# Kernel tuning notes

Measured on AMD Instinct MI355X. Metric: run time of the kernel, lower is better.

The kernel has to match this reference:

```python
import jax, jax.numpy as jnp
import numpy as np

B, T, C, N = 4, 12, 64, 10000
H = 64            # d_inner (GRU hidden)
L = 2             # num_layers
NE = 2000         # number of static hyperedges
NNZ = 80000       # incidence list length
TOPK = 10         # HGCNADP_topk
DE = 16           # HGCNADP_embed_dims
RATE = 0.5        # hyperedge_rate (blend static vs adaptive)


def setup_inputs() -> dict:
    key = jax.random.key(0)
    ks = jax.random.split(key, 10)
    scale = 0.05
    x = jax.random.normal(ks[0], (B, T, C, N), jnp.float32)
    node_idx = jax.random.randint(ks[1], (NNZ,), 0, N, jnp.int32)
    edge_idx = jax.random.randint(ks[2], (NNZ,), 0, NE, jnp.int32)
    hyperedge_index = jnp.stack([node_idx, edge_idx])  # (2, NNZ)
    node_embs = jax.random.normal(ks[3], (L, N, DE), jnp.float32) * 0.1
    W_zr = jax.random.normal(ks[4], (L, C + H, 2 * H), jnp.float32) * scale
    b_zr = jnp.zeros((L, 2 * H), jnp.float32)
    W_c = jax.random.normal(ks[5], (L, C + H, H), jnp.float32) * scale
    b_c = jnp.zeros((L, H), jnp.float32)
    W_out = jax.random.normal(ks[6], (L, H, C), jnp.float32) * scale
    b_out = jnp.zeros((L, C), jnp.float32)
    return {"x": x, "hyperedge_index": hyperedge_index, "node_embs": node_embs,
            "W_zr": W_zr, "b_zr": b_zr, "W_c": W_c, "b_c": b_c,
            "W_out": W_out, "b_out": b_out}


def reference(x, hyperedge_index, node_embs, W_zr, b_zr, W_c, b_c, W_out, b_out):
    # x: (B, T, C, N). Dropout is identity (eval mode).
    node_idx = hyperedge_index[0]
    edge_idx = hyperedge_index[1]
    edge_deg = jnp.zeros((NE,), x.dtype).at[edge_idx].add(1.0)
    inv_e = 1.0 / jnp.maximum(edge_deg, 1.0)
    node_deg = jnp.zeros((N,), x.dtype).at[node_idx].add(1.0)
    inv_n = 1.0 / jnp.maximum(node_deg, 1.0)

    def conv(f, topk_idx, topk_w):
        # f: (B, N, D). Static hypergraph pass: node -> hyperedge -> node.
        msg = jnp.take(f, node_idx, axis=1)                       # (B, NNZ, D)
        eagg = jnp.zeros((f.shape[0], NE, f.shape[2]), f.dtype).at[:, edge_idx].add(msg)
        eagg = eagg * inv_e[None, :, None]                        # (B, NE, D)
        stat = jnp.zeros_like(f).at[:, node_idx].add(jnp.take(eagg, edge_idx, axis=1))
        stat = stat * inv_n[None, :, None]                        # (B, N, D)
        # Adaptive top-k hyperedge aggregation (softmax-weighted neighbor sum).
        adp = jnp.einsum('bnkd,nk->bnd', jnp.take(f, topk_idx, axis=1), topk_w)
        return RATE * stat + (1.0 - RATE) * adp

    out = x
    for l in range(L):
        xl = out.transpose(0, 1, 3, 2)                            # (B, T, N, C)
        E = node_embs[l]
        scores = jax.nn.relu(E @ E.T)                             # (N, N)
        vals, idx = jax.lax.top_k(scores, TOPK)                   # (N, K)
        w = jax.nn.softmax(vals, axis=-1)
        Wz, bz = W_zr[l], b_zr[l]
        Wc_, bc_ = W_c[l], b_c[l]
        Wo, bo = W_out[l], b_out[l]

        def step(h, x_t):
            zr = jax.nn.sigmoid(conv(jnp.concatenate([x_t, h], -1), idx, w) @ Wz + bz)
            z, r = jnp.split(zr, 2, axis=-1)
            c = jnp.tanh(conv(jnp.concatenate([x_t, r * h], -1), idx, w) @ Wc_ + bc_)
            h_new = z * h + (1.0 - z) * c
            return h_new, h_new @ Wo + bo

        h0 = jnp.zeros((out.shape[0], N, H), x.dtype)
        _, ys = jax.lax.scan(step, h0, xl.transpose(1, 0, 2, 3))  # ys: (T, B, N, C)
        out = out + ys.transpose(1, 0, 3, 2)                      # residual, back to (B,T,C,N)
    return out
```

## Files before the change

kernel.cpp:

```cpp
#include <hip/hip_runtime.h>
#include <hip/hip_fp16.h>
#include <cstdio>

#define BB 4
#define TT 12
#define CC 64
#define NN 10000
#define HH 64
#define LL 2
#define NEDGE 2000
#define NNZT 80000
#define KTOP 10
#define DEMB 16
#define BT (BB*TT)

typedef long long ll;
typedef unsigned long long u64;
typedef unsigned int u32;
typedef unsigned short ushort;

typedef short bf16x8 __attribute__((ext_vector_type(8)));
typedef float f32x4 __attribute__((ext_vector_type(4)));

__device__ __forceinline__ void up8(const uint4 v, float* f) {
  const __half2* p = reinterpret_cast<const __half2*>(&v);
  float2 t0 = __half22float2(p[0]);
  float2 t1 = __half22float2(p[1]);
  float2 t2 = __half22float2(p[2]);
  float2 t3 = __half22float2(p[3]);
  f[0]=t0.x; f[1]=t0.y; f[2]=t1.x; f[3]=t1.y;
  f[4]=t2.x; f[5]=t2.y; f[6]=t3.x; f[7]=t3.y;
}
__device__ __forceinline__ uint4 pk8(const float* f) {
  __half2 h0 = __floats2half2_rn(f[0], f[1]);
  __half2 h1 = __floats2half2_rn(f[2], f[3]);
  __half2 h2 = __floats2half2_rn(f[4], f[5]);
  __half2 h3 = __floats2half2_rn(f[6], f[7]);
  uint4 r;
  r.x = *reinterpret_cast<unsigned*>(&h0);
  r.y = *reinterpret_cast<unsigned*>(&h1);
  r.z = *reinterpret_cast<unsigned*>(&h2);
  r.w = *reinterpret_cast<unsigned*>(&h3);
  return r;
}
__device__ __forceinline__ ushort f2bf(float x) {
  u32 u = __float_as_uint(x);
  u32 r = u + 0x7FFFu + ((u >> 16) & 1u);
  return (ushort)(r >> 16);
}
__device__ __forceinline__ uint4 pk8bf(const float* f) {
  uint4 r;
  r.x = (u32)f2bf(f[0]) | ((u32)f2bf(f[1])<<16);
  r.y = (u32)f2bf(f[2]) | ((u32)f2bf(f[3])<<16);
  r.z = (u32)f2bf(f[4]) | ((u32)f2bf(f[5])<<16);
  r.w = (u32)f2bf(f[6]) | ((u32)f2bf(f[7])<<16);
  return r;
}

__global__ void deg_kernel(const int* __restrict__ nidx, const int* __restrict__ eidx,
                           int* __restrict__ ndeg, int* __restrict__ edeg) {
  int i = blockIdx.x*256 + threadIdx.x;
  if (i < NNZT) { atomicAdd(&ndeg[nidx[i]],1); atomicAdd(&edeg[eidx[i]],1); }
}

__global__ void exscan_kernel(const int* __restrict__ cnt, int* __restrict__ off, int n) {
  __shared__ int part[256];
  int tid = threadIdx.x;
  int chunk = (n + 255)/256;
  int lo = tid*chunk, hi = min(lo+chunk, n);
  int s = 0;
  for (int i=lo; i<hi; ++i) s += cnt[i];
  part[tid]=s; __syncthreads();
  if (tid==0){ int acc=0; for(int i=0;i<256;++i){int v=part[i];part[i]=acc;acc+=v;} off[n]=acc; }
  __syncthreads();
  int acc = part[tid];
  for (int i=lo; i<hi; ++i){ off[i]=acc; acc+=cnt[i]; }
}

__global__ void fill_csr_kernel(const int* __restrict__ nidx, const int* __restrict__ eidx,
                                const int* __restrict__ noff, const int* __restrict__ eoff,
                                int* __restrict__ ncur, int* __restrict__ ecur,
                                int* __restrict__ node_edges, int* __restrict__ edge_nodes) {
  int i = blockIdx.x*256 + threadIdx.x;
  if (i >= NNZT) return;
  int n = nidx[i], e = eidx[i];
  int pn = atomicAdd(&ncur[n],1);
  node_edges[noff[n]+pn] = e;
  int pe = atomicAdd(&ecur[e],1);
  edge_nodes[eoff[e]+pe] = n;
}

__global__ void invdeg_kernel(const int* __restrict__ ndeg, const int* __restrict__ edeg,
                              float* __restrict__ inv_n, float* __restrict__ inv_e) {
  int i = blockIdx.x*256+threadIdx.x;
  if (i < NN) inv_n[i] = 1.0f/fmaxf((float)ndeg[i],1.0f);
  if (i < NEDGE) inv_e[i] = 1.0f/fmaxf((float)edeg[i],1.0f);
}

__global__ void prep_w_kernel(const float* __restrict__ W_zr, const float* __restrict__ W_c,
                              const float* __restrict__ W_o,
                              short* __restrict__ Wz_swb, short* __restrict__ Wc_swb,
                              short* __restrict__ Wo_swb) {
  int l = blockIdx.y;
  const float* Wz = W_zr + (size_t)l*128*128;
  const float* Wc = W_c  + (size_t)l*128*64;
  const float* Wo = W_o  + (size_t)l*64*64;
  short* Wz_sw = Wz_swb + (size_t)l*16384;
  short* Wc_sw = Wc_swb + (size_t)l*8192;
  short* Wo_sw = Wo_swb + (size_t)l*4096;
  int idx = blockIdx.x*256 + threadIdx.x;
  if (idx < 16384) {
    int i = idx&7, lane = (idx>>3)&63, kk = (idx>>9)&3, tc = idx>>11;
    int k = kk*32 + (lane>>4)*8 + i, col = tc*16 + (lane&15);
    Wz_sw[idx] = (short)f2bf(Wz[k*128+col]);
  }
  if (idx < 8192) {
    int i = idx&7, lane = (idx>>3)&63, kk = (idx>>9)&3, tc = idx>>11;
    int k = kk*32 + (lane>>4)*8 + i, col = tc*16 + (lane&15);
    Wc_sw[idx] = (short)f2bf(Wc[k*64+col]);
  }
  if (idx < 4096) {
    int i = idx&7, lane = (idx>>3)&63, kk = (idx>>9)&1, tc = idx>>10;
    int k = kk*32 + (lane>>4)*8 + i, col = tc*16 + (lane&15);
    Wo_sw[idx] = (short)f2bf(Wo[k*64+col]);
  }
}

__device__ __forceinline__ u64 sortstep(u64 X, int j, bool dir, int lane) {
  u64 p = __shfl_xor(X, j);
  bool lower = ((lane & j) == 0);
  bool keep_min = (dir == lower);
  bool xlt = (X < p);
  u64 mn = xlt ? X : p;
  u64 mx = xlt ? p : X;
  return keep_min ? mn : mx;
}

__device__ __forceinline__ void reselect(u64* bq, u64& thr, int& cnt, int lane) {
  int tot = 10 + cnt;
  u64 A = (lane < tot)      ? bq[lane]      : 0ull;
  u64 B = (lane + 64 < tot) ? bq[lane + 64] : 0ull;
  for (int k = 2; k <= 32; k <<= 1) {
    for (int j = k >> 1; j >= 1; j >>= 1) {
      bool dir = ((lane & k) == 0);
      A = sortstep(A, j, dir, lane);
      B = sortstep(B, j, dir, lane);
    }
  }
  for (int j = 32; j >= 1; j >>= 1) {
    A = sortstep(A, j, true,  lane);
    B = sortstep(B, j, false, lane);
  }
  {
    bool lt = (A < B);
    u64 mn = lt ? A : B, mx = lt ? B : A;
    A = mn; B = mx;
  }
  for (int j = 32; j >= 1; j >>= 1) {
    A = sortstep(A, j, true, lane);
    B = sortstep(B, j, true, lane);
  }
  if (lane >= 54) bq[63 - lane] = B;
  thr = __shfl(B, 54);
  cnt = 0;
}

__global__ void __launch_bounds__(256) topk_kernel(const float* __restrict__ embs,
                                                   int* __restrict__ tk_idx_b,
                                                   float* __restrict__ tk_w_b) {
  __shared__ u64 buf[16][128];
  const float* E = embs + (ll)blockIdx.y*NN*DEMB;
  int* tk_idx = tk_idx_b + (ll)blockIdx.y*NN*KTOP;
  float* tk_w = tk_w_b + (ll)blockIdx.y*NN*KTOP;
  int tid = threadIdx.x;
  int wv = tid >> 6, lane = tid & 63;
  int qbase = blockIdx.x*16 + wv*4;
  const float4* E4 = (const float4*)E;
  float4 q[4][4];
  #pragma unroll
  for (int u=0;u<4;++u) {
    int n = qbase + u;
    #pragma unroll
    for (int j=0;j<4;++j) q[u][j] = E4[(ll)n*4 + j];
  }
  u64 thr[4] = {0,0,0,0};
  int cnt[4] = {0,0,0,0};
  buf[tid>>4][tid&15] = 0ull;
  for (int cb=0; cb<NN; cb+=64) {
    int cand = cb + lane;
    bool valid = (cand < NN);
    int ca = valid ? cand : 0;
    float4 a0 = E4[(ll)ca*4], a1 = E4[(ll)ca*4+1], a2 = E4[(ll)ca*4+2], a3 = E4[(ll)ca*4+3];
    u64 low = (u64)(0x00FFFFFFu - (unsigned)cand);
    u64 key[4];
    #pragma unroll
    for (int u=0;u<4;++u) {
      float dot = q[u][0].x*a0.x + q[u][0].y*a0.y + q[u][0].z*a0.z + q[u][0].w*a0.w
                + q[u][1].x*a1.x + q[u][1].y*a1.y + q[u][1].z*a1.z + q[u][1].w*a1.w
                + q[u][2].x*a2.x + q[u][2].y*a2.y + q[u][2].z*a2.z + q[u][2].w*a2.w
                + q[u][3].x*a3.x + q[u][3].y*a3.y + q[u][3].z*a3.z + q[u][3].w*a3.w;
      float s = fmaxf(dot, 0.f);
      u64 kk = ((u64)__float_as_uint(s) << 32) | low;
      key[u] = valid ? kk : 0ull;
    }
    #pragma unroll
    for (int u=0;u<4;++u) {
      u64 mask = __ballot(key[u] > thr[u]);
      if (mask) {
        if (key[u] > thr[u]) {
          int myofs = (int)__popcll(mask & ((1ull<<lane)-1ull));
          buf[wv*4+u][10 + cnt[u] + myofs] = key[u];
        }
        cnt[u] += (int)__popcll(mask);
        if (cnt[u] >= 40) reselect(&buf[wv*4+u][0], thr[u], cnt[u], lane);
      }
    }
  }
  #pragma unroll
  for (int u=0;u<4;++u) {
    u64* bq = &buf[wv*4+u][0];
    if (cnt[u] > 0) reselect(bq, thr[u], cnt[u], lane);
    u64 k10 = (lane < 10) ? bq[lane] : 0ull;
    float v = __uint_as_float((unsigned)(k10 >> 32));
    int idx = 0x00FFFFFF - (int)(k10 & 0xFFFFFFFFull);
    float v0 = __shfl(v, 0);
    float e = (lane < 10) ? expf(v - v0) : 0.f;
    float s = e;
    for (int o=1;o<16;o<<=1) s += __shfl_xor(s, o);
    if (lane < 10) {
      int n = qbase + u;
      tk_w[n*KTOP + lane] = e / s;
      tk_idx[n*KTOP + lane] = idx;
    }
  }
}

__global__ void transpose_kernel(const float* __restrict__ src, __half* __restrict__ dst) {
  __shared__ float tile[32][33];
  int bt = blockIdx.z;
  int n0 = blockIdx.x*32, c0 = blockIdx.y*32;
  for (int i=threadIdx.y; i<32; i+=8) {
    int c = c0+i, nn = n0+threadIdx.x;
    tile[i][threadIdx.x] = (nn<NN)? src[((ll)bt*CC + c)*NN + nn] : 0.0f;
  }
  __syncthreads();
  for (int i=threadIdx.y; i<32; i+=8) {
    int nn = n0+i, c = c0+threadIdx.x;
    if (nn<NN) dst[((ll)bt*NN+nn)*64 + c] = __float2half_rn(tile[threadIdx.x][i]);
  }
}

__global__ void __launch_bounds__(256) edge_agg_kernel(
    const uint4* __restrict__ f8, uint4* __restrict__ eagg8,
    const int* __restrict__ eoff, const int* __restrict__ enodes,
    const float* __restrict__ inv_e) {
  __shared__ int en_s[1088];
  __shared__ int jo_s[17];
  int tid = threadIdx.x;
  int e0 = blockIdx.x*16;
  int s = blockIdx.y;
  if (tid < 17) jo_s[tid] = eoff[e0 + tid];
  __syncthreads();
  int jb0 = jo_s[0], cnt = jo_s[16] - jb0;
  bool stg = (cnt <= 1088);
  if (stg) for (int i = tid; i < cnt; i += 256) en_s[i] = enodes[jb0 + i];
  __syncthreads();
  int esub = tid>>4;
  int e = e0 + esub;
  int hsel = (tid>>3)&1;
  int lane8 = tid&7;
  int j0 = jo_s[esub] - jb0, j1 = jo_s[esub+1] - jb0;
  const uint4* fb = f8 + (ll)s*NN*8;
  float acc[8] = {0,0,0,0,0,0,0,0};
  for (int j = j0 + hsel; j < j1; j += 2) {
    int node = stg ? en_s[j] : enodes[jb0+j];
    float t[8]; up8(fb[(ll)node*8 + lane8], t);
    #pragma unroll
    for (int q=0;q<8;++q) acc[q] += t[q];
  }
  #pragma unroll
  for (int q=0;q<8;++q) acc[q] += __shfl_xor(acc[q], 8);
  if (hsel == 0) {
    float sc = inv_e[e];
    #pragma unroll
    for (int q=0;q<8;++q) acc[q] *= sc;
    eagg8[((ll)s*NEDGE+e)*8 + lane8] = pk8(acc);
  }
}

__global__ void __launch_bounds__(256) conv_x_kernel(
    const uint4* __restrict__ xt8, const uint4* __restrict__ eagg8,
    const int* __restrict__ noff, const int* __restrict__ nedges,
    const float* __restrict__ inv_n,
    const int* __restrict__ tk_idx, const float* __restrict__ tk_w,
    uint4* __restrict__ cx8) {
  __shared__ int tki_s[32][KTOP];
  __shared__ float tkw_s[32][KTOP];
  __shared__ int ne_s[640];
  __shared__ int no_s[33];
  int tid = threadIdx.x; int s = blockIdx.y; int n0 = blockIdx.x*32;
  if (tid < 33) no_s[tid] = noff[min(n0 + tid, NN)];
  for (int i=tid; i<32*KTOP; i+=256) {
    int r=i/KTOP, k=i%KTOP; int n = n0+r;
    tki_s[r][k] = (n<NN)? tk_idx[n*KTOP+k] : 0;
    tkw_s[r][k] = (n<NN)? tk_w[n*KTOP+k] : 0.f;
  }
  __syncthreads();
  int jb0 = no_s[0], cnt = no_s[32] - jb0;
  bool stg = (cnt <= 640);
  if (stg) for (int i=tid; i<cnt; i+=256) ne_s[i] = nedges[jb0+i];
  __syncthreads();
  int row = tid>>3, lane8 = tid&7;
  int n = n0 + row;
  if (n >= NN) return;
  float stv[8] = {0,0,0,0,0,0,0,0};
  const uint4* eb = eagg8 + (ll)s*NEDGE*8;
  int j0 = no_s[row] - jb0, j1 = no_s[row+1] - jb0;
  for (int j=j0;j<j1;++j) {
    int eidx = stg ? ne_s[j] : nedges[jb0+j];
    float t[8]; up8(eb[(ll)eidx*8 + lane8], t);
    #pragma unroll
    for (int q=0;q<8;++q) stv[q] += t[q];
  }
  float sc = 0.5f*inv_n[n];
  float adv[8] = {0,0,0,0,0,0,0,0};
  const uint4* xb = xt8 + (ll)s*NN*8;
  #pragma unroll
  for (int k=0;k<KTOP;++k) {
    float w = tkw_s[row][k];
    float t[8]; up8(xb[(ll)tki_s[row][k]*8 + lane8], t);
    #pragma unroll
    for (int q=0;q<8;++q) adv[q] += w*t[q];
  }
  float r8[8];
  #pragma unroll
  for (int q=0;q<8;++q) r8[q] = sc*stv[q] + 0.5f*adv[q];
  cx8[((ll)s*NN+n)*8+lane8] = pk8(r8);
}

__global__ void __launch_bounds__(256) step0_kernel(
    const uint4* __restrict__ cx8,
    const short* __restrict__ Wz_sw, const float* __restrict__ bz,
    const short* __restrict__ Wc_sw, const float* __restrict__ bc,
    const short* __restrict__ Wo_sw, const float* __restrict__ bo,
    __half* __restrict__ h, float* __restrict__ out) {
  __shared__ __align__(16) short in_bf[32][72];
  __shared__ __align__(16) short hn[32][72];
  __shared__ __align__(16) float yt[64][36];
  int tid = threadIdx.x;
  int b = blockIdx.y; int n0 = blockIdx.x*32;
  int bt = b*TT;
  {
    int row = tid>>3, lane8 = tid&7;
    int n = n0 + row;
    float cxv[8] = {0,0,0,0,0,0,0,0};
    if (n < NN) up8(cx8[((ll)bt*NN + n)*8 + lane8], cxv);
    *(uint4*)&in_bf[row][lane8*8] = pk8bf(cxv);
  }
  __syncthreads();
  int wv = tid>>6, lane = tid&63;
  int m = lane&15, g = lane>>4;
  #pragma unroll
  for (int q=0;q<2;++q) {
    int T = wv + 4*q;
    int tr = T>>2, tc = T&3;
    f32x4 az = {0.f,0.f,0.f,0.f};
    f32x4 ac = {0.f,0.f,0.f,0.f};
    #pragma unroll
    for (int kk=0;kk<2;++kk) {
      bf16x8 a = *(const bf16x8*)&in_bf[tr*16 + m][kk*32 + g*8];
      bf16x8 bwz = *(const bf16x8*)&Wz_sw[((tc*4+kk)*64 + lane)*8];
      bf16x8 bwc = *(const bf16x8*)&Wc_sw[((tc*4+kk)*64 + lane)*8];
      az = __builtin_amdgcn_mfma_f32_16x16x32_bf16(a, bwz, az, 0, 0, 0);
      ac = __builtin_amdgcn_mfma_f32_16x16x32_bf16(a, bwc, ac, 0, 0, 0);
    }
    int col = tc*16 + m;
    float bzv = bz[col], bcv = bc[col];
    #pragma unroll
    for (int r=0;r<4;++r) {
      int row = tr*16 + g*4 + r;
      int n = n0 + row;
      float z = 1.0f/(1.0f+expf(-(az[r]+bzv)));
      float cval = tanhf(ac[r]+bcv);
      float hnew = (1.0f-z)*cval;
      if (n < NN) h[((ll)b*NN+n)*64+col] = __float2half_rn(hnew);
      hn[row][col] = (short)f2bf(hnew);
    }
  }
  __syncthreads();
  #pragma unroll
  for (int q=0;q<2;++q) {
    int T = wv + 4*q;
    int tr = T>>2, tc = T&3;
    f32x4 acc = {0.f,0.f,0.f,0.f};
    #pragma unroll
    for (int kk=0;kk<2;++kk) {
      bf16x8 a = *(const bf16x8*)&hn[tr*16 + m][kk*32 + g*8];
      bf16x8 bw = *(const bf16x8*)&Wo_sw[((tc*2+kk)*64 + lane)*8];
      acc = __builtin_amdgcn_mfma_f32_16x16x32_bf16(a, bw, acc, 0, 0, 0);
    }
    int col = tc*16 + m;
    float bias = bo[col];
    #pragma unroll
    for (int r=0;r<4;++r) {
      int row = tr*16 + g*4 + r;
      yt[col][row] = acc[r] + bias;
    }
  }
  __syncthreads();
  #pragma unroll
  for (int kk=0;kk<2;++kk) {
    int slot = tid + kk*256;
    int col = slot>>3, q = slot&7;
    int n = n0 + q*4;
    if (n < NN) {
      float4 y = *(const float4*)&yt[col][q*4];
      float4* dst = (float4*)&out[((ll)bt*64+col)*NN + n];
      float4 cur = *dst;
      cur.x += y.x; cur.y += y.y; cur.z += y.z; cur.w += y.w;
      *dst = cur;
    }
  }
}

__global__ void __launch_bounds__(256) step_zr_kernel(
    const uint4* __restrict__ h8, const uint4* __restrict__ cx8,
    const uint4* __restrict__ eagg8,
    const short* __restrict__ Wz_sw, const float* __restrict__ bz,
    const int* __restrict__ noff, const int* __restrict__ nedges,
    const float* __restrict__ inv_n,
    const int* __restrict__ tk_idx, const float* __restrict__ tk_w,
    const __half* __restrict__ hs,
    __half* __restrict__ rh, __half* __restrict__ zout, int t) {
  __shared__ __align__(16) short in_bf[32][136];
  __shared__ int tki_s[32][KTOP];
  __shared__ float tkw_s[32][KTOP];
  __shared__ int ne_s[640];
  __shared__ int no_s[33];
  int tid = threadIdx.x;
  int b = blockIdx.y; int n0 = blockIdx.x*32;
  int bt = b*TT + t;
  if (tid < 33) no_s[tid] = noff[min(n0 + tid, NN)];
  for (int i=tid; i<32*KTOP; i+=256) {
    int r=i/KTOP, k=i%KTOP; int n=n0+r;
    tki_s[r][k] = (n<NN)? tk_idx[n*KTOP+k] : 0;
    tkw_s[r][k] = (n<NN)? tk_w[n*KTOP+k] : 0.f;
  }
  __syncthreads();
  int jb0 = no_s[0], ecnt = no_s[32] - jb0;
  bool stg = (ecnt <= 640);
  if (stg) for (int i=tid; i<ecnt; i+=256) ne_s[i] = nedges[jb0+i];
  __syncthreads();
  {
    int row = tid>>3, lane8 = tid&7;
    int n = n0 + row;
    float cxv[8] = {0,0,0,0,0,0,0,0};
    float chv[8] = {0,0,0,0,0,0,0,0};
    if (n < NN) {
      up8(cx8[((ll)bt*NN + n)*8 + lane8], cxv);
      float stv[8] = {0,0,0,0,0,0,0,0};
      int j0 = no_s[row] - jb0, j1 = no_s[row+1] - jb0;
      const uint4* eb = eagg8 + (ll)b*NEDGE*8;
      for (int j=j0;j<j1;++j) {
        int eidx = stg ? ne_s[j] : nedges[jb0+j];
        float t8[8]; up8(eb[(ll)eidx*8 + lane8], t8);
        #pragma unroll
        for (int q=0;q<8;++q) stv[q] += t8[q];
      }
      float sc = 0.5f*inv_n[n];
      const uint4* hb = h8 + (ll)b*NN*8;
      float adv[8] = {0,0,0,0,0,0,0,0};
      #pragma unroll
      for (int k=0;k<KTOP;++k) {
        float w = tkw_s[row][k];
        float t8[8]; up8(hb[(ll)tki_s[row][k]*8 + lane8], t8);
        #pragma unroll
        for (int q=0;q<8;++q) adv[q] += w*t8[q];
      }
      #pragma unroll
      for (int q=0;q<8;++q) chv[q] = sc*stv[q] + 0.5f*adv[q];
    }
    *(uint4*)&in_bf[row][lane8*8]    = pk8bf(cxv);
    *(uint4*)&in_bf[row][64+lane8*8] = pk8bf(chv);
  }
  __syncthreads();
  int wv = tid>>6, lane = tid&63;
  int m = lane&15, g = lane>>4;
  #pragma unroll
  for (int q=0;q<4;++q) {
    int T = wv*4 + q;
    int tr = T>>3, tc = T&7;
    f32x4 acc = {0.f,0.f,0.f,0.f};
    #pragma unroll
    for (int kk=0;kk<4;++kk) {
      bf16x8 a = *(const bf16x8*)&in_bf[tr*16 + m][kk*32 + g*8];
      bf16x8 bf = *(const bf16x8*)&Wz_sw[((tc*4+kk)*64 + lane)*8];
      acc = __builtin_amdgcn_mfma_f32_16x16x32_bf16(a, bf, acc, 0, 0, 0);
    }
    int col = tc*16 + m;
    float bias = bz[col];
    #pragma unroll
    for (int r=0;r<4;++r) {
      int row = tr*16 + g*4 + r;
      int n = n0 + row;
      if (n < NN) {
        float v = 1.0f/(1.0f+expf(-(acc[r]+bias)));
        if (col < 64) zout[((ll)b*NN+n)*64+col] = __float2half_rn(v);
        else {
          int c = col-64;
          float hv = __half2float(hs[((ll)b*NN+n)*64+c]);
          rh[((ll)b*NN+n)*64+c] = __float2half_rn(v*hv);
        }
      }
    }
  }
}

__global__ void __launch_bounds__(256) step_hy_kernel(
    const uint4* __restrict__ rh8, const uint4* __restrict__ cx8,
    const uint4* __restrict__ eagg8,
    const short* __restrict__ Wc_sw, const float* __restrict__ bc,
    const short* __restrict__ Wo_sw, const float* __restrict__ bo,
    const int* __restrict__ noff, const int* __restrict__ nedges,
    const float* __restrict__ inv_n,
    const int* __restrict__ tk_idx, const float* __restrict__ tk_w,
    const __half* __restrict__ zbuf, __half* __restrict__ h,
    float* __restrict__ out, int t) {
  __shared__ __align__(16) short in_bf[32][136];
  __shared__ __align__(16) short hn[32][72];
  __shared__ __align__(16) float yt[64][36];
  __shared__ int tki_s[32][KTOP];
  __shared__ float tkw_s[32][KTOP];
  __shared__ int ne_s[640];
  __shared__ int no_s[33];
  int tid = threadIdx.x;
  int b = blockIdx.y; int n0 = blockIdx.x*32;
  int bt = b*TT + t;
  if (tid < 33) no_s[tid] = noff[min(n0 + tid, NN)];
  for (int i=tid; i<32*KTOP; i+=256) {
    int r=i/KTOP, k=i%KTOP; int n=n0+r;
    tki_s[r][k] = (n<NN)? tk_idx[n*KTOP+k] : 0;
    tkw_s[r][k] = (n<NN)? tk_w[n*KTOP+k] : 0.f;
  }
  __syncthreads();
  int jb0 = no_s[0], ecnt = no_s[32] - jb0;
  bool stg = (ecnt <= 640);
  if (stg) for (int i=tid; i<ecnt; i+=256) ne_s[i] = nedges[jb0+i];
  __syncthreads();
  {
    int row = tid>>3, lane8 = tid&7;
    int n = n0 + row;
    float cxv[8] = {0,0,0,0,0,0,0,0};
    float chv[8] = {0,0,0,0,0,0,0,0};
    if (n < NN) {
      up8(cx8[((ll)bt*NN + n)*8 + lane8], cxv);
      float stv[8] = {0,0,0,0,0,0,0,0};
      int j0 = no_s[row] - jb0, j1 = no_s[row+1] - jb0;
      const uint4* eb = eagg8 + (ll)b*NEDGE*8;
      for (int j=j0;j<j1;++j) {
        int eidx = stg ? ne_s[j] : nedges[jb0+j];
        float t8[8]; up8(eb[(ll)eidx*8 + lane8], t8);
        #pragma unroll
        for (int q=0;q<8;++q) stv[q] += t8[q];
      }
      float sc = 0.5f*inv_n[n];
      const uint4* rb = rh8 + (ll)b*NN*8;
      float adv[8] = {0,0,0,0,0,0,0,0};
      #pragma unroll
      for (int k=0;k<KTOP;++k) {
        float w = tkw_s[row][k];
        float t8[8]; up8(rb[(ll)tki_s[row][k]*8 + lane8], t8);
        #pragma unroll
        for (int q=0;q<8;++q) adv[q] += w*t8[q];
      }
      #pragma unroll
      for (int q=0;q<8;++q) chv[q] = sc*stv[q] + 0.5f*adv[q];
    }
    *(uint4*)&in_bf[row][lane8*8]    = pk8bf(cxv);
    *(uint4*)&in_bf[row][64+lane8*8] = pk8bf(chv);
  }
  __syncthreads();
  int wv = tid>>6, lane = tid&63;
  int m = lane&15, g = lane>>4;
  #pragma unroll
  for (int q=0;q<2;++q) {
    int T = wv + 4*q;
    int tr = T>>2, tc = T&3;
    f32x4 acc = {0.f,0.f,0.f,0.f};
    #pragma unroll
    for (int kk=0;kk<4;++kk) {
      bf16x8 a = *(const bf16x8*)&in_bf[tr*16 + m][kk*32 + g*8];
      bf16x8 bf = *(const bf16x8*)&Wc_sw[((tc*4+kk)*64 + lane)*8];
      acc = __builtin_amdgcn_mfma_f32_16x16x32_bf16(a, bf, acc, 0, 0, 0);
    }
    int col = tc*16 + m;
    float bias = bc[col];
    #pragma unroll
    for (int r=0;r<4;++r) {
      int row = tr*16 + g*4 + r;
      int n = n0 + row;
      float hnew = 0.0f;
      if (n < NN) {
        float cval = tanhf(acc[r]+bias);
        float z = __half2float(zbuf[((ll)b*NN+n)*64+col]);
        float hv = __half2float(h[((ll)b*NN+n)*64+col]);
        hnew = z*hv + (1.0f-z)*cval;
        h[((ll)b*NN+n)*64+col] = __float2half_rn(hnew);
      }
      hn[row][col] = (short)f2bf(hnew);
    }
  }
  __syncthreads();
  #pragma unroll
  for (int q=0;q<2;++q) {
    int T = wv + 4*q;
    int tr = T>>2, tc = T&3;
    f32x4 acc = {0.f,0.f,0.f,0.f};
    #pragma unroll
    for (int kk=0;kk<2;++kk) {
      bf16x8 a = *(const bf16x8*)&hn[tr*16 + m][kk*32 + g*8];
      bf16x8 bf = *(const bf16x8*)&Wo_sw[((tc*2+kk)*64 + lane)*8];
      acc = __builtin_amdgcn_mfma_f32_16x16x32_bf16(a, bf, acc, 0, 0, 0);
    }
    int col = tc*16 + m;
    float bias = bo[col];
    #pragma unroll
    for (int r=0;r<4;++r) {
      int row = tr*16 + g*4 + r;
      yt[col][row] = acc[r] + bias;
    }
  }
  __syncthreads();
  #pragma unroll
  for (int kk=0;kk<2;++kk) {
    int slot = tid + kk*256;
    int col = slot>>3, q = slot&7;
    int n = n0 + q*4;
    if (n < NN) {
      float4 y = *(const float4*)&yt[col][q*4];
      float4* dst = (float4*)&out[((ll)bt*64+col)*NN + n];
      float4 cur = *dst;
      cur.x += y.x; cur.y += y.y; cur.z += y.z; cur.w += y.w;
      *dst = cur;
    }
  }
}

extern "C" void kernel_launch(void* const* d_in, const int* in_sizes, int n_in,
                              void* d_out, int out_size, void* d_ws, size_t ws_size,
                              hipStream_t stream) {
  const float* x    = (const float*)d_in[0];
  const int*  hidx  = (const int*)d_in[1];
  const float* embs = (const float*)d_in[2];
  const float* W_zr = (const float*)d_in[3];
  const float* b_zr = (const float*)d_in[4];
  const float* W_c  = (const float*)d_in[5];
  const float* b_c  = (const float*)d_in[6];
  const float* W_out= (const float*)d_in[7];
  const float* b_out= (const float*)d_in[8];
  const int* node_idx = hidx;
  const int* edge_idx = hidx + NNZT;

  char* ws = (char*)d_ws;
  size_t off = 0;
  auto alloc = [&](size_t bytes) -> void* {
    void* p = ws + off; off += (bytes + 255) & ~(size_t)255; return p;
  };
  __half* xt    = (__half*)alloc((size_t)BT*NN*64*2);
  __half* cx    = (__half*)alloc((size_t)BT*NN*64*2);
  __half* eaggx = (__half*)alloc((size_t)BT*NEDGE*64*2);
  __half* eaggh = (__half*)alloc((size_t)BB*NEDGE*64*2);
  __half* hbuf  = (__half*)alloc((size_t)BB*NN*64*2);
  __half* rhbuf = (__half*)alloc((size_t)BB*NN*64*2);
  __half* zbuf  = (__half*)alloc((size_t)BB*NN*64*2);
  short* Wz_sw = (short*)alloc((size_t)LL*16384*2);
  short* Wc_sw = (short*)alloc((size_t)LL*8192*2);
  short* Wo_sw = (short*)alloc((size_t)LL*4096*2);
  float* tkw   = (float*)alloc((size_t)LL*NN*KTOP*4);
  float* inv_e = (float*)alloc(NEDGE*4);
  float* inv_n = (float*)alloc(NN*4);
  int* tki     = (int*)alloc((size_t)LL*NN*KTOP*4);
  int* ndeg    = (int*)alloc(NN*4);
  int* edeg    = (int*)alloc(NEDGE*4);
  int* noff    = (int*)alloc((NN+1)*4);
  int* eoff    = (int*)alloc((NEDGE+1)*4);
  int* ncur    = (int*)alloc(NN*4);
  int* ecur    = (int*)alloc(NEDGE*4);
  int* nedges  = (int*)alloc(NNZT*4);
  int* enodes  = (int*)alloc(NNZT*4);
  if (off > ws_size) {
    fprintf(stderr, "kernel_launch: ws too small, need %zu have %zu\n", off, ws_size);
    return;
  }

  hipMemcpyAsync(d_out, x, (size_t)BB*TT*CC*NN*4, hipMemcpyDeviceToDevice, stream);

  hipMemsetAsync(ndeg, 0, NN*4, stream);
  hipMemsetAsync(edeg, 0, NEDGE*4, stream);
  hipMemsetAsync(ncur, 0, NN*4, stream);
  hipMemsetAsync(ecur, 0, NEDGE*4, stream);
  deg_kernel<<<(NNZT+255)/256,256,0,stream>>>(node_idx, edge_idx, ndeg, edeg);
  exscan_kernel<<<1,256,0,stream>>>(ndeg, noff, NN);
  exscan_kernel<<<1,256,0,stream>>>(edeg, eoff, NEDGE);
  fill_csr_kernel<<<(NNZT+255)/256,256,0,stream>>>(node_idx, edge_idx, noff, eoff,
                                                   ncur, ecur, nedges, enodes);
  invdeg_kernel<<<(NN+255)/256,256,0,stream>>>(ndeg, edeg, inv_n, inv_e);

  prep_w_kernel<<<dim3(64,LL),256,0,stream>>>(W_zr, W_c, W_out, Wz_sw, Wc_sw, Wo_sw);
  topk_kernel<<<dim3(625,LL),256,0,stream>>>(embs, tki, tkw);

  float* outp = (float*)d_out;
  for (int l=0; l<LL; ++l) {
    const short* Wzs = Wz_sw + (size_t)l*16384;
    const short* Wcs = Wc_sw + (size_t)l*8192;
    const short* Wos = Wo_sw + (size_t)l*4096;
    const float* bz = b_zr + l*128;
    const float* bc = b_c + l*64;
    const float* bo = b_out + l*64;
    const int* tkil = tki + (size_t)l*NN*KTOP;
    const float* tkwl = tkw + (size_t)l*NN*KTOP;
    transpose_kernel<<<dim3((NN+31)/32, CC/32, BT), dim3(32,8), 0, stream>>>(outp, xt);
    edge_agg_kernel<<<dim3(125, BT),256,0,stream>>>(
        (const uint4*)xt, (uint4*)eaggx, eoff, enodes, inv_e);
    conv_x_kernel<<<dim3(313, BT),256,0,stream>>>(
        (const uint4*)xt, (const uint4*)eaggx, noff, nedges, inv_n, tkil, tkwl, (uint4*)cx);
    step0_kernel<<<dim3(313, BB),256,0,stream>>>(
        (const uint4*)cx, Wzs, bz, Wcs, bc, Wos, bo, hbuf, outp);
    for (int t=1; t<TT; ++t) {
      edge_agg_kernel<<<dim3(125, BB),256,0,stream>>>(
          (const uint4*)hbuf, (uint4*)eaggh, eoff, enodes, inv_e);
      step_zr_kernel<<<dim3(313, BB),256,0,stream>>>(
          (const uint4*)hbuf, (const uint4*)cx, (const uint4*)eaggh, Wzs, bz,
          noff, nedges, inv_n, tkil, tkwl, hbuf, rhbuf, zbuf, t);
      edge_agg_kernel<<<dim3(125, BB),256,0,stream>>>(
          (const uint4*)rhbuf, (uint4*)eaggh, eoff, enodes, inv_e);
      step_hy_kernel<<<dim3(313, BB),256,0,stream>>>(
          (const uint4*)rhbuf, (const uint4*)cx, (const uint4*)eaggh, Wcs, bc, Wos, bo,
          noff, nedges, inv_n, tkil, tkwl, zbuf, hbuf, outp, t);
    }
  }
}
```

Baseline: 2.588 ms.

## Merge top-k with first transpose, pack top-k pairs, store cx as bf16

Combines the top-k selection and the layer-0 transpose into one launch so the long-running top-k blocks can overlap with the bandwidth-bound transpose blocks. The top-k filter now compares float scores against a float threshold before building 64-bit keys, which cuts per-candidate work. Index and weight are packed into one int2 array so each neighbor needs a single load. cx is written directly in bf16 so the step kernels copy it without converting. The merged kernel reserves 16KB of shared memory for every block, which may lower occupancy for the transpose blocks. The inclusive >= threshold test can also admit more candidates and trigger extra reselects.

```diff
diff --git a/kernel.cpp b/kernel.cpp
--- a/kernel.cpp
+++ b/kernel.cpp
@@ -13,6 +13,8 @@
 #define KTOP 10
 #define DEMB 16
 #define BT (BB*TT)
+#define TOPK_BLKS 1250
+#define TRN_BLKS 30048
 
 typedef long long ll;
 typedef unsigned long long u64;
@@ -165,16 +167,14 @@
   cnt = 0;
 }
 
-__global__ void __launch_bounds__(256) topk_kernel(const float* __restrict__ embs,
-                                                   int* __restrict__ tk_idx_b,
-                                                   float* __restrict__ tk_w_b) {
-  __shared__ u64 buf[16][128];
-  const float* E = embs + (ll)blockIdx.y*NN*DEMB;
-  int* tk_idx = tk_idx_b + (ll)blockIdx.y*NN*KTOP;
-  float* tk_w = tk_w_b + (ll)blockIdx.y*NN*KTOP;
+__device__ void topk_body(int layer, int qb, char* smem,
+                          const float* __restrict__ embs, int2* __restrict__ tkc_b) {
+  u64 (*buf)[128] = (u64(*)[128])smem;
+  const float* E = embs + (ll)layer*NN*DEMB;
+  int2* tkc = tkc_b + (ll)layer*NN*KTOP;
   int tid = threadIdx.x;
   int wv = tid >> 6, lane = tid & 63;
-  int qbase = blockIdx.x*16 + wv*4;
+  int qbase = qb*16 + wv*4;
   const float4* E4 = (const float4*)E;
   float4 q[4][4];
   #pragma unroll
@@ -184,6 +184,7 @@
     for (int j=0;j<4;++j) q[u][j] = E4[(ll)n*4 + j];
   }
   u64 thr[4] = {0,0,0,0};
+  float thrf[4] = {0.f,0.f,0.f,0.f};
   int cnt[4] = {0,0,0,0};
   buf[tid>>4][tid&15] = 0ull;
   for (int cb=0; cb<NN; cb+=64) {
@@ -192,7 +193,7 @@
     int ca = valid ? cand : 0;
     float4 a0 = E4[(ll)ca*4], a1 = E4[(ll)ca*4+1], a2 = E4[(ll)ca*4+2], a3 = E4[(ll)ca*4+3];
     u64 low = (u64)(0x00FFFFFFu - (unsigned)cand);
-    u64 key[4];
+    float sv[4];
     #pragma unroll
     for (int u=0;u<4;++u) {
       float dot = q[u][0].x*a0.x + q[u][0].y*a0.y + q[u][0].z*a0.z + q[u][0].w*a0.w
@@ -200,19 +201,22 @@
                 + q[u][2].x*a2.x + q[u][2].y*a2.y + q[u][2].z*a2.z + q[u][2].w*a2.w
                 + q[u][3].x*a3.x + q[u][3].y*a3.y + q[u][3].z*a3.z + q[u][3].w*a3.w;
       float s = fmaxf(dot, 0.f);
-      u64 kk = ((u64)__float_as_uint(s) << 32) | low;
-      key[u] = valid ? kk : 0ull;
+      sv[u] = valid ? s : -1.f;
     }
     #pragma unroll
     for (int u=0;u<4;++u) {
-      u64 mask = __ballot(key[u] > thr[u]);
+      u64 mask = __ballot(sv[u] >= thrf[u]);
       if (mask) {
-        if (key[u] > thr[u]) {
+        if (sv[u] >= thrf[u]) {
+          u64 key = ((u64)__float_as_uint(sv[u]) << 32) | low;
           int myofs = (int)__popcll(mask & ((1ull<<lane)-1ull));
-          buf[wv*4+u][10 + cnt[u] + myofs] = key[u];
+          buf[wv*4+u][10 + cnt[u] + myofs] = key;
         }
         cnt[u] += (int)__popcll(mask);
-        if (cnt[u] >= 40) reselect(&buf[wv*4+u][0], thr[u], cnt[u], lane);
+        if (cnt[u] >= 40) {
+          reselect(&buf[wv*4+u][0], thr[u], cnt[u], lane);
+          thrf[u] = __uint_as_float((u32)(thr[u] >> 32));
+        }
       }
     }
   }
@@ -229,25 +233,44 @@
     for (int o=1;o<16;o<<=1) s += __shfl_xor(s, o);
     if (lane < 10) {
       int n = qbase + u;
-      tk_w[n*KTOP + lane] = e / s;
-      tk_idx[n*KTOP + lane] = idx;
-    }
-  }
+      tkc[n*KTOP + lane] = make_int2(idx, __float_as_int(e / s));
+    }
+  }
+}
+
+__device__ void transpose_body(int tb, char* smem,
+                               const float* __restrict__ src, __half* __restrict__ dst) {
+  float (*tile)[33] = (float(*)[33])smem;
+  int tid = threadIdx.x;
+  int tx = tid & 31, ty = tid >> 5;
+  int bt = tb / 626;
+  int rem = tb % 626;
+  int n0 = (rem % 313)*32, c0 = (rem/313)*32;
+  for (int i=ty; i<32; i+=8) {
+    int c = c0+i, nn = n0+tx;
+    tile[i][tx] = (nn<NN)? src[((ll)bt*CC + c)*NN + nn] : 0.0f;
+  }
+  __syncthreads();
+  for (int i=ty; i<32; i+=8) {
+    int nn = n0+i, c = c0+tx;
+    if (nn<NN) dst[((ll)bt*NN+nn)*64 + c] = __float2half_rn(tile[tx][i]);
+  }
+}
+
+__global__ void __launch_bounds__(256) mega1_kernel(const float* __restrict__ embs,
+                                                    int2* __restrict__ tkc,
+                                                    const float* __restrict__ x,
+                                                    __half* __restrict__ xt) {
+  __shared__ __align__(16) char smem[16384];
+  int bid = blockIdx.x;
+  if (bid < TOPK_BLKS) topk_body(bid/625, bid%625, smem, embs, tkc);
+  else transpose_body(bid - TOPK_BLKS, smem, x, xt);
 }
 
 __global__ void transpose_kernel(const float* __restrict__ src, __half* __restrict__ dst) {
-  __shared__ float tile[32][33];
-  int bt = blockIdx.z;
-  int n0 = blockIdx.x*32, c0 = blockIdx.y*32;
-  for (int i=threadIdx.y; i<32; i+=8) {
-    int c = c0+i, nn = n0+threadIdx.x;
-    tile[i][threadIdx.x] = (nn<NN)? src[((ll)bt*CC + c)*NN + nn] : 0.0f;
-  }
-  __syncthreads();
-  for (int i=threadIdx.y; i<32; i+=8) {
-    int nn = n0+i, c = c0+threadIdx.x;
-    if (nn<NN) dst[((ll)bt*NN+nn)*64 + c] = __float2half_rn(tile[threadIdx.x][i]);
-  }
+  __shared__ __align__(16) char smem[4352];
+  int tb = (blockIdx.z*626) + blockIdx.y*313 + blockIdx.x;
+  transpose_body(tb, smem, src, dst);
 }
 
 __global__ void __launch_bounds__(256) edge_agg_kernel(
@@ -292,7 +315,7 @@
     const uint4* __restrict__ xt8, const uint4* __restrict__ eagg8,
     const int* __restrict__ noff, const int* __restrict__ nedges,
     const float* __restrict__ inv_n,
-    const int* __restrict__ tk_idx, const float* __restrict__ tk_w,
+    const int2* __restrict__ tkc,
     uint4* __restrict__ cx8) {
   __shared__ int tki_s[32][KTOP];
   __shared__ float tkw_s[32][KTOP];
@@ -302,8 +325,9 @@
   if (tid < 33) no_s[tid] = noff[min(n0 + tid, NN)];
   for (int i=tid; i<32*KTOP; i+=256) {
     int r=i/KTOP, k=i%KTOP; int n = n0+r;
-    tki_s[r][k] = (n<NN)? tk_idx[n*KTOP+k] : 0;
-    tkw_s[r][k] = (n<NN)? tk_w[n*KTOP+k] : 0.f;
+    int2 p = (n<NN)? tkc[n*KTOP+k] : make_int2(0,0);
+    tki_s[r][k] = p.x;
+    tkw_s[r][k] = __int_as_float(p.y);
   }
   __syncthreads();
   int jb0 = no_s[0], cnt = no_s[32] - jb0;
@@ -335,7 +359,7 @@
   float r8[8];
   #pragma unroll
   for (int q=0;q<8;++q) r8[q] = sc*stv[q] + 0.5f*adv[q];
-  cx8[((ll)s*NN+n)*8+lane8] = pk8(r8);
+  cx8[((ll)s*NN+n)*8+lane8] = pk8bf(r8);
 }
 
 __global__ void __launch_bounds__(256) step0_kernel(
@@ -353,9 +377,9 @@
   {
     int row = tid>>3, lane8 = tid&7;
     int n = n0 + row;
-    float cxv[8] = {0,0,0,0,0,0,0,0};
-    if (n < NN) up8(cx8[((ll)bt*NN + n)*8 + lane8], cxv);
-    *(uint4*)&in_bf[row][lane8*8] = pk8bf(cxv);
+    uint4 cxv4 = make_uint4(0,0,0,0);
+    if (n < NN) cxv4 = cx8[((ll)bt*NN + n)*8 + lane8];
+    *(uint4*)&in_bf[row][lane8*8] = cxv4;
   }
   __syncthreads();
   int wv = tid>>6, lane = tid&63;
@@ -429,7 +453,7 @@
     const short* __restrict__ Wz_sw, const float* __restrict__ bz,
     const int* __restrict__ noff, const int* __restrict__ nedges,
     const float* __restrict__ inv_n,
-    const int* __restrict__ tk_idx, const float* __restrict__ tk_w,
+    const int2* __restrict__ tkc,
     const __half* __restrict__ hs,
     __half* __restrict__ rh, __half* __restrict__ zout, int t) {
   __shared__ __align__(16) short in_bf[32][136];
@@ -443,8 +467,9 @@
   if (tid < 33) no_s[tid] = noff[min(n0 + tid, NN)];
   for (int i=tid; i<32*KTOP; i+=256) {
     int r=i/KTOP, k=i%KTOP; int n=n0+r;
-    tki_s[r][k] = (n<NN)? tk_idx[n*KTOP+k] : 0;
-    tkw_s[r][k] = (n<NN)? tk_w[n*KTOP+k] : 0.f;
+    int2 p = (n<NN)? tkc[n*KTOP+k] : make_int2(0,0);
+    tki_s[r][k] = p.x;
+    tkw_s[r][k] = __int_as_float(p.y);
   }
   __syncthreads();
   int jb0 = no_s[0], ecnt = no_s[32] - jb0;
@@ -454,10 +479,10 @@
   {
     int row = tid>>3, lane8 = tid&7;
     int n = n0 + row;
-    float cxv[8] = {0,0,0,0,0,0,0,0};
+    uint4 cxv4 = make_uint4(0,0,0,0);
     float chv[8] = {0,0,0,0,0,0,0,0};
     if (n < NN) {
-      up8(cx8[((ll)bt*NN + n)*8 + lane8], cxv);
+      cxv4 = cx8[((ll)bt*NN + n)*8 + lane8];
       float stv[8] = {0,0,0,0,0,0,0,0};
       int j0 = no_s[row] - jb0, j1 = no_s[row+1] - jb0;
       const uint4* eb = eagg8 + (ll)b*NEDGE*8;
@@ -480,7 +505,7 @@
       #pragma unroll
       for (int q=0;q<8;++q) chv[q] = sc*stv[q] + 0.5f*adv[q];
     }
-    *(uint4*)&in_bf[row][lane8*8]    = pk8bf(cxv);
+    *(uint4*)&in_bf[row][lane8*8]    = cxv4;
     *(uint4*)&in_bf[row][64+lane8*8] = pk8bf(chv);
   }
   __syncthreads();
@@ -523,7 +548,7 @@
     const short* __restrict__ Wo_sw, const float* __restrict__ bo,
     const int* __restrict__ noff, const int* __restrict__ nedges,
     const float* __restrict__ inv_n,
-    const int* __restrict__ tk_idx, const float* __restrict__ tk_w,
+    const int2* __restrict__ tkc,
     const __half* __restrict__ zbuf, __half* __restrict__ h,
     float* __restrict__ out, int t) {
   __shared__ __align__(16) short in_bf[32][136];
@@ -539,8 +564,9 @@
   if (tid < 33) no_s[tid] = noff[min(n0 + tid, NN)];
   for (int i=tid; i<32*KTOP; i+=256) {
     int r=i/KTOP, k=i%KTOP; int n=n0+r;
-    tki_s[r][k] = (n<NN)? tk_idx[n*KTOP+k] : 0;
-    tkw_s[r][k] = (n<NN)? tk_w[n*KTOP+k] : 0.f;
+    int2 p = (n<NN)? tkc[n*KTOP+k] : make_int2(0,0);
+    tki_s[r][k] = p.x;
+    tkw_s[r][k] = __int_as_float(p.y);
   }
   __syncthreads();
   int jb0 = no_s[0], ecnt = no_s[32] - jb0;
@@ -550,10 +576,10 @@
   {
     int row = tid>>3, lane8 = tid&7;
     int n = n0 + row;
-    float cxv[8] = {0,0,0,0,0,0,0,0};
+    uint4 cxv4 = make_uint4(0,0,0,0);
     float chv[8] = {0,0,0,0,0,0,0,0};
     if (n < NN) {
-      up8(cx8[((ll)bt*NN + n)*8 + lane8], cxv);
+      cxv4 = cx8[((ll)bt*NN + n)*8 + lane8];
       float stv[8] = {0,0,0,0,0,0,0,0};
       int j0 = no_s[row] - jb0, j1 = no_s[row+1] - jb0;
       const uint4* eb = eagg8 + (ll)b*NEDGE*8;
@@ -576,7 +602,7 @@
       #pragma unroll
       for (int q=0;q<8;++q) chv[q] = sc*stv[q] + 0.5f*adv[q];
     }
-    *(uint4*)&in_bf[row][lane8*8]    = pk8bf(cxv);
+    *(uint4*)&in_bf[row][lane8*8]    = cxv4;
     *(uint4*)&in_bf[row][64+lane8*8] = pk8bf(chv);
   }
   __syncthreads();
@@ -676,10 +702,9 @@
   short* Wz_sw = (short*)alloc((size_t)LL*16384*2);
   short* Wc_sw = (short*)alloc((size_t)LL*8192*2);
   short* Wo_sw = (short*)alloc((size_t)LL*4096*2);
-  float* tkw   = (float*)alloc((size_t)LL*NN*KTOP*4);
+  int2* tkc    = (int2*)alloc((size_t)LL*NN*KTOP*8);
   float* inv_e = (float*)alloc(NEDGE*4);
   float* inv_n = (float*)alloc(NN*4);
-  int* tki     = (int*)alloc((size_t)LL*NN*KTOP*4);
   int* ndeg    = (int*)alloc(NN*4);
   int* edeg    = (int*)alloc(NEDGE*4);
   int* noff    = (int*)alloc((NN+1)*4);
@@ -707,9 +732,9 @@
   invdeg_kernel<<<(NN+255)/256,256,0,stream>>>(ndeg, edeg, inv_n, inv_e);
 
   prep_w_kernel<<<dim3(64,LL),256,0,stream>>>(W_zr, W_c, W_out, Wz_sw, Wc_sw, Wo_sw);
-  topk_kernel<<<dim3(625,LL),256,0,stream>>>(embs, tki, tkw);
-
   float* outp = (float*)d_out;
+  mega1_kernel<<<TOPK_BLKS + TRN_BLKS,256,0,stream>>>(embs, tkc, outp, xt);
+
   for (int l=0; l<LL; ++l) {
     const short* Wzs = Wz_sw + (size_t)l*16384;
     const short* Wcs = Wc_sw + (size_t)l*8192;
@@ -717,13 +742,13 @@
     const float* bz = b_zr + l*128;
     const float* bc = b_c + l*64;
     const float* bo = b_out + l*64;
-    const int* tkil = tki + (size_t)l*NN*KTOP;
-    const float* tkwl = tkw + (size_t)l*NN*KTOP;
-    transpose_kernel<<<dim3((NN+31)/32, CC/32, BT), dim3(32,8), 0, stream>>>(outp, xt);
+    const int2* tkcl = tkc + (size_t)l*NN*KTOP;
+    if (l > 0)
+      transpose_kernel<<<dim3(313, 2, BT), 256, 0, stream>>>(outp, xt);
     edge_agg_kernel<<<dim3(125, BT),256,0,stream>>>(
         (const uint4*)xt, (uint4*)eaggx, eoff, enodes, inv_e);
     conv_x_kernel<<<dim3(313, BT),256,0,stream>>>(
-        (const uint4*)xt, (const uint4*)eaggx, noff, nedges, inv_n, tkil, tkwl, (uint4*)cx);
+        (const uint4*)xt, (const uint4*)eaggx, noff, nedges, inv_n, tkcl, (uint4*)cx);
     step0_kernel<<<dim3(313, BB),256,0,stream>>>(
         (const uint4*)cx, Wzs, bz, Wcs, bc, Wos, bo, hbuf, outp);
     for (int t=1; t<TT; ++t) {
@@ -731,12 +756,12 @@
           (const uint4*)hbuf, (uint4*)eaggh, eoff, enodes, inv_e);
       step_zr_kernel<<<dim3(313, BB),256,0,stream>>>(
           (const uint4*)hbuf, (const uint4*)cx, (const uint4*)eaggh, Wzs, bz,
-          noff, nedges, inv_n, tkil, tkwl, hbuf, rhbuf, zbuf, t);
+          noff, nedges, inv_n, tkcl, hbuf, rhbuf, zbuf, t);
       edge_agg_kernel<<<dim3(125, BB),256,0,stream>>>(
           (const uint4*)rhbuf, (uint4*)eaggh, eoff, enodes, inv_e);
       step_hy_kernel<<<dim3(313, BB),256,0,stream>>>(
           (const uint4*)rhbuf, (const uint4*)cx, (const uint4*)eaggh, Wcs, bc, Wos, bo,
-          noff, nedges, inv_n, tkil, tkwl, zbuf, hbuf, outp, t);
-    }
-  }
-}
+          noff, nedges, inv_n, tkcl, zbuf, hbuf, outp, t);
+    }
+  }
+}
```

New measurement: 2.354 ms. 9.1% less time.
